# Performance work log

Hardware: AMD Instinct MI355X
Metric: run time of the kernel (lower is better)

## Reference

```python
import jax, jax.numpy as jnp
import numpy as np
import math

D_MODEL = 512
EXPAND = 1
D_INNER = EXPAND * D_MODEL          # 512
HALF = D_INNER // 2                 # 256 per-branch channels
D_STATE = D_MODEL // 4 * EXPAND     # 128 (overrides d_state arg in __init__)
DT_RANK = math.ceil(D_MODEL / 16)   # 32
D_CONV = 4


def _dwconv_same(x, w):
    # x: (B, C, L), w: (C, 1, k); torch padding='same' for k=4 -> pad (left=1, right=2)
    k = w.shape[-1]
    total = k - 1
    left = total // 2
    return jax.lax.conv_general_dilated(
        x, w, window_strides=(1,), padding=[(left, total - left)],
        feature_group_count=w.shape[0], dimension_numbers=("NCH", "OIH", "NCH"))


def _sparse_approx(m):
    thr = jnp.max(m) * 0.1
    return jnp.sign(m) * jax.nn.relu(jnp.abs(m) - thr)


def _selective_scan(u, delta, A, Bc, Cc, D):
    # u, delta: (B, d, L); A: (d, n); Bc, Cc: (B, n, L); D: (d,)
    dT = jnp.moveaxis(delta, 2, 0)   # (L, B, d)
    uT = jnp.moveaxis(u, 2, 0)       # (L, B, d)
    BT = jnp.moveaxis(Bc, 2, 0)      # (L, B, n)
    CT = jnp.moveaxis(Cc, 2, 0)      # (L, B, n)

    def step(h, inputs):
        d_t, u_t, b_t, c_t = inputs                      # (B,d),(B,d),(B,n),(B,n)
        dA = jnp.exp(d_t[..., None] * A)                 # (B, d, n)
        dBu = d_t[..., None] * b_t[:, None, :] * u_t[..., None]
        h = dA * h + dBu                                 # (B, d, n)
        y = jnp.einsum("bdn,bn->bd", h, c_t)
        return h, y

    h0 = jnp.zeros((u.shape[0], u.shape[1], A.shape[1]), dtype=u.dtype)
    _, ys = jax.lax.scan(step, h0, (dT, uT, BT, CT))     # ys: (L, B, d)
    y = jnp.moveaxis(ys, 0, 2)                           # (B, d, L)
    return y + u * D[:, None]


def _branch(inph, in_w, cx_w, cz_w, xproj_w, dt_w, dt_b, out_w, A, D):
    # inph: (B, L, d_model)
    xz = jnp.swapaxes(inph @ in_w.T, 1, 2)   # (B, d_inner, L)
    x, z = xz[:, :HALF], xz[:, HALF:]
    x = jax.nn.silu(_dwconv_same(x, cx_w))   # (B, half, L); conv bias is False (True//2==0)
    z = jax.nn.silu(_dwconv_same(z, cz_w))
    x_dbl = jnp.swapaxes(x, 1, 2) @ xproj_w.T        # (B, L, dt_rank + 2n)
    dt = x_dbl[..., :DT_RANK] @ dt_w.T               # (B, L, half)
    dt = jnp.swapaxes(dt, 1, 2)                      # (B, half, L)
    Bc = jnp.swapaxes(x_dbl[..., DT_RANK:DT_RANK + D_STATE], 1, 2)   # (B, n, L)
    Cc = jnp.swapaxes(x_dbl[..., DT_RANK + D_STATE:], 1, 2)          # (B, n, L)
    Bc = _sparse_approx(Bc)
    Cc = _sparse_approx(Cc)
    delta = jax.nn.softplus(dt + dt_b[None, :, None])
    y = _selective_scan(x, delta, A, Bc, Cc, D)
    out = jnp.concatenate([y, z], axis=1)            # (B, d_inner, L)
    return jnp.swapaxes(out, 1, 2) @ out_w.T         # (B, L, d_model)


def setup_inputs() -> dict:
    key = jax.random.key(0)
    ks = jax.random.split(key, 16)
    B, L = 2, 2048
    s = lambda fan: 1.0 / np.sqrt(fan)

    inp = jax.random.normal(ks[0], (B, 2 * D_MODEL, L), jnp.float32)

    in_proj_w = jax.random.uniform(ks[1], (D_INNER, D_MODEL), jnp.float32, -s(D_MODEL), s(D_MODEL))
    x_proj_w = jax.random.uniform(ks[2], (DT_RANK + 2 * D_STATE, HALF), jnp.float32, -s(HALF), s(HALF))
    dt_init_std = DT_RANK ** (-0.5)
    dt_proj_w = jax.random.uniform(ks[3], (HALF, DT_RANK), jnp.float32, -dt_init_std, dt_init_std)
    out_proj_w = jax.random.uniform(ks[4], (D_MODEL, D_INNER), jnp.float32, -s(D_INNER), s(D_INNER))

    in_proj_2_w = jax.random.uniform(ks[5], (D_INNER, D_MODEL), jnp.float32, -s(D_MODEL), s(D_MODEL))
    x_proj_2_w = jax.random.uniform(ks[6], (DT_RANK + 2 * D_STATE, HALF), jnp.float32, -s(HALF), s(HALF))
    dt_proj_2_w = jax.random.uniform(ks[7], (HALF, DT_RANK), jnp.float32, -dt_init_std, dt_init_std)
    out_proj_2_w = jax.random.uniform(ks[8], (D_MODEL, D_INNER), jnp.float32, -s(D_INNER), s(D_INNER))

    # dt bias init: inverse-softplus of dt ~ LogUniform(1e-3, 1e-1), floor 1e-4
    def inv_softplus_dt(k):
        u = jax.random.uniform(k, (HALF,), jnp.float32)
        dt = jnp.exp(u * (np.log(0.1) - np.log(0.001)) + np.log(0.001))
        dt = jnp.clip(dt, 1e-4, None)
        return dt + jnp.log(-jnp.expm1(-dt))
    dt_proj_b = inv_softplus_dt(ks[9])
    dt_proj_2_b = inv_softplus_dt(ks[10])

    cs = 1.0 / np.sqrt(D_CONV)  # depthwise conv fan_in = 1*k
    conv_x_w = jax.random.uniform(ks[11], (HALF, 1, D_CONV), jnp.float32, -cs, cs)
    conv_z_w = jax.random.uniform(ks[12], (HALF, 1, D_CONV), jnp.float32, -cs, cs)
    conv_x_2_w = jax.random.uniform(ks[13], (HALF, 1, D_CONV), jnp.float32, -cs, cs)
    conv_z_2_w = jax.random.uniform(ks[14], (HALF, 1, D_CONV), jnp.float32, -cs, cs)

    A_log = jnp.log(jnp.broadcast_to(jnp.arange(1, D_STATE + 1, dtype=jnp.float32), (HALF, D_STATE)))
    D = jnp.ones((HALF,), jnp.float32)
    epsilon = jnp.array([0.01], jnp.float32)

    return dict(inp=inp, in_proj_w=in_proj_w, conv_x_w=conv_x_w, conv_z_w=conv_z_w,
                x_proj_w=x_proj_w, dt_proj_w=dt_proj_w, dt_proj_b=dt_proj_b, out_proj_w=out_proj_w,
                in_proj_2_w=in_proj_2_w, conv_x_2_w=conv_x_2_w, conv_z_2_w=conv_z_2_w,
                x_proj_2_w=x_proj_2_w, dt_proj_2_w=dt_proj_2_w, dt_proj_2_b=dt_proj_2_b,
                out_proj_2_w=out_proj_2_w, A_log=A_log, D=D, epsilon=epsilon)


def reference(inp, in_proj_w, conv_x_w, conv_z_w, x_proj_w, dt_proj_w, dt_proj_b, out_proj_w,
              in_proj_2_w, conv_x_2_w, conv_z_2_w, x_proj_2_w, dt_proj_2_w, dt_proj_2_b,
              out_proj_2_w, A_log, D, epsilon):
    # inp: (B, 2*d_model, L) -> split along dim 1, permute to (B, L, d_model)
    inpx = jnp.swapaxes(inp[:, :D_MODEL, :], 1, 2)
    inpy = jnp.swapaxes(inp[:, D_MODEL:, :], 1, 2)

    A_base = (1.0 + epsilon[0]) * (-jnp.exp(A_log))
    A1 = _sparse_approx(A_base)        # branch 1
    A2 = _sparse_approx(A1)            # branch 2 sparsifies the already-sparsified A

    out1 = _branch(inpx, in_proj_w, conv_x_w, conv_z_w, x_proj_w, dt_proj_w, dt_proj_b, out_proj_w, A1, D)
    out2 = _branch(inpy, in_proj_2_w, conv_x_2_w, conv_z_2_w, x_proj_2_w, dt_proj_2_w, dt_proj_2_b, out_proj_2_w, A2, D)
    return out1, out2
```

## Files before the change

### kernel.cpp

```cpp
#include <hip/hip_runtime.h>
#include <math.h>

constexpr int B_    = 2;
constexpr int L_    = 2048;
constexpr int NROW  = B_ * L_;
constexpr int MROW  = 2 * NROW;
constexpr int HALF_ = 256;
constexpr int DS_   = 128;

constexpr float LOG2E = 1.4426950408889634f;

constexpr size_t OFF_MINP = 0;
constexpr size_t OFF_BCMX = 32;
constexpr size_t OFF_XZ   = 64;
constexpr size_t OFF_YT   = OFF_XZ + (size_t)MROW * 256;
constexpr size_t OFF_XDBL = OFF_XZ + (size_t)MROW * 512;
constexpr size_t OFF_XS   = OFF_XDBL + (size_t)MROW * 288;
constexpr size_t OFF_BS   = OFF_XS  + (size_t)MROW * 256;
constexpr size_t OFF_CS   = OFF_BS  + (size_t)2 * NROW * 128;
constexpr size_t OFF_DTT  = OFF_CS  + (size_t)2 * NROW * 128;
constexpr size_t OFF_DUT  = OFF_DTT + (size_t)2 * 256 * 4096;
constexpr size_t OFF_UDT  = OFF_DUT + (size_t)2 * 256 * 4096;
constexpr size_t FLOAT_END = OFF_UDT + (size_t)2 * 256 * 4096;

constexpr size_t HOFF_XINH = 0;
constexpr size_t HOFF_XINL = HOFF_XINH + (size_t)MROW * 512;
constexpr size_t HOFF_YZH  = HOFF_XINH;
constexpr size_t HOFF_YZL  = HOFF_XINL;
constexpr size_t HOFF_XSH  = HOFF_XINL + (size_t)MROW * 512;
constexpr size_t HOFF_XSL  = HOFF_XSH  + (size_t)MROW * 256;
constexpr size_t HOFF_INWH = HOFF_XSL  + (size_t)MROW * 256;
constexpr size_t HOFF_INWL = HOFF_INWH + 524288;
constexpr size_t HOFF_XWH  = HOFF_INWL + 524288;
constexpr size_t HOFF_XWL  = HOFF_XWH  + 147456;
constexpr size_t HOFF_OUTWH= HOFF_XWL  + 147456;
constexpr size_t HOFF_OUTWL= HOFF_OUTWH+ 524288;

constexpr size_t WST_IN = 262144;
constexpr size_t WST_X  = 73728;

constexpr int PRE_MINA = 32;
constexpr int PRE_WSPL = (1196032 + 255) / 256;
constexpr int PRE_TIN  = 64 * 16 * 4;
constexpr int PRE_BLOCKS = PRE_MINA + PRE_WSPL + PRE_TIN;

typedef __bf16 bf16x8 __attribute__((ext_vector_type(8)));
typedef float  f32x4  __attribute__((ext_vector_type(4)));

__device__ __forceinline__ unsigned short bf16rn(float x) {
    unsigned u = __float_as_uint(x);
    unsigned r = (u + 0x7FFFu + ((u >> 16) & 1u)) >> 16;
    return (unsigned short)r;
}
__device__ __forceinline__ void split2(float x, unsigned short& h, unsigned short& l) {
    h = bf16rn(x);
    float hf = __uint_as_float(((unsigned)h) << 16);
    l = bf16rn(x - hf);
}

__device__ __forceinline__ float shrinkf(float v, float thr) {
    float a = fabsf(v) - thr;
    a = fmaxf(a, 0.0f);
    float r = copysignf(a, v);
    return (v == 0.0f) ? 0.0f : r;
}
__device__ __forceinline__ float siluf(float v) { return v / (1.0f + __expf(-v)); }
__device__ __forceinline__ float softplusf(float v) {
    return fmaxf(v, 0.0f) + log1pf(__expf(-fabsf(v)));
}
__device__ __forceinline__ float rlanef(float v, int l) {
    return __int_as_float(__builtin_amdgcn_readlane(__float_as_int(v), l));
}
__device__ __forceinline__ unsigned fkey(float f) {
    unsigned u = __float_as_uint(f);
    return (u >> 31) ? ~u : (u | 0x80000000u);
}
__device__ __forceinline__ float funkey(unsigned k) {
    unsigned u = (k >> 31) ? (k & 0x7FFFFFFFu) : ~k;
    return __uint_as_float(u);
}

__global__ __launch_bounds__(256) void pre_all(const float* __restrict__ A_log,
                                               const float* __restrict__ inp,
                                               const float* __restrict__ in_w0,
                                               const float* __restrict__ in_w1,
                                               const float* __restrict__ outw0,
                                               const float* __restrict__ outw1,
                                               const float* __restrict__ xw0,
                                               const float* __restrict__ xw1,
                                               float* __restrict__ ws,
                                               unsigned* __restrict__ bcmax,
                                               unsigned short* __restrict__ hb) {
    int bid = blockIdx.x;
    int tid = threadIdx.x;
    if (bid < PRE_MINA) {
        __shared__ float sbuf[8];
        int i = bid * 1024 + tid * 4;
        float4 v = *(const float4*)(A_log + i);
        float mv = fminf(fminf(v.x, v.y), fminf(v.z, v.w));
        #pragma unroll
        for (int off = 32; off > 0; off >>= 1) mv = fminf(mv, __shfl_xor(mv, off));
        if ((tid & 63) == 0) sbuf[tid >> 6] = mv;
        __syncthreads();
        if (tid == 0) {
            float r = fminf(fminf(sbuf[0], sbuf[1]), fminf(sbuf[2], sbuf[3]));
            ws[OFF_MINP + bid] = r;
        }
        if (bid == 0 && tid < 4) bcmax[tid] = 0u;
    } else if (bid < PRE_MINA + PRE_WSPL) {
        int i = (bid - PRE_MINA) * 256 + tid;
        if (i >= 1196032) return;
        const float* src;
        size_t hbase, lbase;
        int off;
        if (i < 1048576) {
            int t = i >> 18;
            off = i & 262143;
            src = (t == 0) ? in_w0 : (t == 1) ? in_w1 : (t == 2) ? outw0 : outw1;
            if (t < 2) { hbase = HOFF_INWH + (size_t)t * WST_IN;  lbase = HOFF_INWL + (size_t)t * WST_IN; }
            else       { hbase = HOFF_OUTWH + (size_t)(t - 2) * WST_IN; lbase = HOFF_OUTWL + (size_t)(t - 2) * WST_IN; }
        } else {
            int j = i - 1048576;
            int t = (j < (int)WST_X) ? 0 : 1;
            off = j - t * (int)WST_X;
            src = t ? xw1 : xw0;
            hbase = HOFF_XWH + (size_t)t * WST_X;
            lbase = HOFF_XWL + (size_t)t * WST_X;
        }
        unsigned short h, l;
        split2(src[off], h, l);
        hb[hbase + off] = h;
        hb[lbase + off] = l;
    } else {
        __shared__ float tile[32][33];
        int idx = bid - PRE_MINA - PRE_WSPL;
        int bx = idx & 63;
        int by = (idx >> 6) & 15;
        int z  = idx >> 10;
        int br = z >> 1;
        int b  = z & 1;
        int t0 = bx * 32;
        int m0 = by * 32;
        int tx = tid & 31;
        int ty = tid >> 5;
        #pragma unroll
        for (int k = 0; k < 4; k++) {
            tile[ty + 8 * k][tx] =
                inp[((size_t)b * 1024 + br * 512 + m0 + ty + 8 * k) * L_ + t0 + tx];
        }
        __syncthreads();
        #pragma unroll
        for (int k = 0; k < 4; k++) {
            size_t dst = ((size_t)br * NROW + (size_t)b * L_ + t0 + ty + 8 * k) * 512 + m0 + tx;
            unsigned short h, l;
            split2(tile[tx][ty + 8 * k], h, l);
            hb[HOFF_XINH + dst] = h;
            hb[HOFF_XINL + dst] = l;
        }
    }
}

template <int NGUARD, int DOMAX>
__global__ __launch_bounds__(256) void gemm_mfma(const unsigned short* __restrict__ Ah,
                                                 const unsigned short* __restrict__ Al, int lda,
                                                 const unsigned short* __restrict__ WhB,
                                                 const unsigned short* __restrict__ WlB,
                                                 size_t wstride,
                                                 float* __restrict__ C, int ldc,
                                                 int N, int K,
                                                 unsigned* __restrict__ bcmax) {
    __shared__ __align__(16) unsigned short sAh[128 * 40];
    __shared__ __align__(16) unsigned short sAl[128 * 40];
    __shared__ __align__(16) unsigned short sBh[64 * 40];
    __shared__ __align__(16) unsigned short sBl[64 * 40];
    int tid  = threadIdx.x;
    int wid  = tid >> 6;
    int lane = tid & 63;
    int fr   = lane & 15;
    int kg   = lane >> 4;
    int mblk = blockIdx.y * 128;
    int nblk = blockIdx.x * 64;
    int br   = (mblk >= NROW) ? 1 : 0;
    const unsigned short* Wh = WhB + (size_t)br * wstride;
    const unsigned short* Wl = WlB + (size_t)br * wstride;
    int srow = tid >> 2;
    int skp  = (tid & 3) * 8;
    bool brow_ok = (!NGUARD) || ((nblk + srow) < N);

    const unsigned short* pA0 = Ah + (size_t)(mblk + srow) * lda + skp;
    const unsigned short* pA1 = Ah + (size_t)(mblk + 64 + srow) * lda + skp;
    const unsigned short* pL0 = Al + (size_t)(mblk + srow) * lda + skp;
    const unsigned short* pL1 = Al + (size_t)(mblk + 64 + srow) * lda + skp;
    const unsigned short* pBh = Wh + (size_t)(nblk + srow) * K + skp;
    const unsigned short* pBl = Wl + (size_t)(nblk + srow) * K + skp;

    f32x4 acc[2][4] = {};

    uint4 rah0 = *(const uint4*)(pA0);
    uint4 rah1 = *(const uint4*)(pA1);
    uint4 ral0 = *(const uint4*)(pL0);
    uint4 ral1 = *(const uint4*)(pL1);
    uint4 rbh = {0, 0, 0, 0}, rbl = {0, 0, 0, 0};
    if (brow_ok) {
        rbh = *(const uint4*)(pBh);
        rbl = *(const uint4*)(pBl);
    }

    for (int k0 = 0; k0 < K; k0 += 32) {
        __syncthreads();
        *(uint4*)(sAh + srow * 40 + skp) = rah0;
        *(uint4*)(sAh + (64 + srow) * 40 + skp) = rah1;
        *(uint4*)(sAl + srow * 40 + skp) = ral0;
        *(uint4*)(sAl + (64 + srow) * 40 + skp) = ral1;
        *(uint4*)(sBh + srow * 40 + skp) = rbh;
        *(uint4*)(sBl + srow * 40 + skp) = rbl;
        __syncthreads();

        int kn = k0 + 32;
        if (kn < K) {
            rah0 = *(const uint4*)(pA0 + kn);
            rah1 = *(const uint4*)(pA1 + kn);
            ral0 = *(const uint4*)(pL0 + kn);
            ral1 = *(const uint4*)(pL1 + kn);
            if (brow_ok) {
                rbh = *(const uint4*)(pBh + kn);
                rbl = *(const uint4*)(pBl + kn);
            }
        }

        bf16x8 ah0 = *(const bf16x8*)(sAh + (wid * 32 + fr) * 40 + kg * 8);
        bf16x8 ah1 = *(const bf16x8*)(sAh + (wid * 32 + 16 + fr) * 40 + kg * 8);
        bf16x8 al0 = *(const bf16x8*)(sAl + (wid * 32 + fr) * 40 + kg * 8);
        bf16x8 al1 = *(const bf16x8*)(sAl + (wid * 32 + 16 + fr) * 40 + kg * 8);
        #pragma unroll
        for (int nt = 0; nt < 4; nt++) {
            bf16x8 bh = *(const bf16x8*)(sBh + (nt * 16 + fr) * 40 + kg * 8);
            bf16x8 bl = *(const bf16x8*)(sBl + (nt * 16 + fr) * 40 + kg * 8);
            acc[0][nt] = __builtin_amdgcn_mfma_f32_16x16x32_bf16(ah0, bh, acc[0][nt], 0, 0, 0);
            acc[0][nt] = __builtin_amdgcn_mfma_f32_16x16x32_bf16(ah0, bl, acc[0][nt], 0, 0, 0);
            acc[0][nt] = __builtin_amdgcn_mfma_f32_16x16x32_bf16(al0, bh, acc[0][nt], 0, 0, 0);
            acc[1][nt] = __builtin_amdgcn_mfma_f32_16x16x32_bf16(ah1, bh, acc[1][nt], 0, 0, 0);
            acc[1][nt] = __builtin_amdgcn_mfma_f32_16x16x32_bf16(ah1, bl, acc[1][nt], 0, 0, 0);
            acc[1][nt] = __builtin_amdgcn_mfma_f32_16x16x32_bf16(al1, bh, acc[1][nt], 0, 0, 0);
        }
    }
    #pragma unroll
    for (int mt = 0; mt < 2; mt++) {
        #pragma unroll
        for (int nt = 0; nt < 4; nt++) {
            int col = nblk + nt * 16 + fr;
            if (NGUARD && col >= N) continue;
            #pragma unroll
            for (int r = 0; r < 4; r++) {
                int row = mblk + wid * 32 + mt * 16 + kg * 4 + r;
                C[(size_t)row * ldc + col] = acc[mt][nt][r];
            }
        }
    }
    if (DOMAX) {
        float mb = -INFINITY, mc = -INFINITY;
        #pragma unroll
        for (int nt = 0; nt < 4; nt++) {
            int c16 = nblk + nt * 16;
            if (c16 >= 32 && c16 < 160) {
                #pragma unroll
                for (int mt = 0; mt < 2; mt++)
                    #pragma unroll
                    for (int r = 0; r < 4; r++) mb = fmaxf(mb, acc[mt][nt][r]);
            } else if (c16 >= 160 && c16 < 288) {
                #pragma unroll
                for (int mt = 0; mt < 2; mt++)
                    #pragma unroll
                    for (int r = 0; r < 4; r++) mc = fmaxf(mc, acc[mt][nt][r]);
            }
        }
        #pragma unroll
        for (int off = 32; off > 0; off >>= 1) {
            mb = fmaxf(mb, __shfl_xor(mb, off));
            mc = fmaxf(mc, __shfl_xor(mc, off));
        }
        if (lane == 0) {
            if (mb > -INFINITY) atomicMax(bcmax + 2 * br,     fkey(mb));
            if (mc > -INFINITY) atomicMax(bcmax + 2 * br + 1, fkey(mc));
        }
    }
}

__global__ __launch_bounds__(256) void conv_silu_kernel(const float* __restrict__ xz,
                                                        float* __restrict__ xs,
                                                        unsigned short* __restrict__ xsh,
                                                        unsigned short* __restrict__ xsl,
                                                        unsigned short* __restrict__ yzh,
                                                        unsigned short* __restrict__ yzl,
                                                        const float* __restrict__ wx0,
                                                        const float* __restrict__ wx1,
                                                        const float* __restrict__ wz0,
                                                        const float* __restrict__ wz1) {
    int gid = blockIdx.x * 256 + threadIdx.x;
    int c4  = (gid & 63) << 2;
    int row = gid >> 6;
    int br  = row >> 12;
    int t   = row & (L_ - 1);
    const float* wx = br ? wx1 : wx0;
    const float* wz = br ? wz1 : wz0;
    float4 wxv[4], wzv[4];
    #pragma unroll
    for (int k = 0; k < 4; k++) {
        wxv[k] = *(const float4*)(wx + (c4 + k) * 4);
        wzv[k] = *(const float4*)(wz + (c4 + k) * 4);
    }
    float4 ax = {0, 0, 0, 0}, az = {0, 0, 0, 0};
    #pragma unroll
    for (int j = 0; j < 4; j++) {
        int tt = t + j - 1;
        if (tt >= 0 && tt < L_) {
            const float* p = xz + (size_t)(row + j - 1) * 512;
            float4 vx = *(const float4*)(p + c4);
            float4 vz = *(const float4*)(p + 256 + c4);
            ax.x = fmaf(vx.x, ((const float*)&wxv[0])[j], ax.x);
            ax.y = fmaf(vx.y, ((const float*)&wxv[1])[j], ax.y);
            ax.z = fmaf(vx.z, ((const float*)&wxv[2])[j], ax.z);
            ax.w = fmaf(vx.w, ((const float*)&wxv[3])[j], ax.w);
            az.x = fmaf(vz.x, ((const float*)&wzv[0])[j], az.x);
            az.y = fmaf(vz.y, ((const float*)&wzv[1])[j], az.y);
            az.z = fmaf(vz.z, ((const float*)&wzv[2])[j], az.z);
            az.w = fmaf(vz.w, ((const float*)&wzv[3])[j], az.w);
        }
    }
    float4 sx, sz;
    sx.x = siluf(ax.x); sx.y = siluf(ax.y); sx.z = siluf(ax.z); sx.w = siluf(ax.w);
    sz.x = siluf(az.x); sz.y = siluf(az.y); sz.z = siluf(az.z); sz.w = siluf(az.w);
    *(float4*)(xs + (size_t)row * 256 + c4) = sx;
    ushort4 hx, lx, hz, lz;
    split2(sx.x, hx.x, lx.x); split2(sx.y, hx.y, lx.y);
    split2(sx.z, hx.z, lx.z); split2(sx.w, hx.w, lx.w);
    split2(sz.x, hz.x, lz.x); split2(sz.y, hz.y, lz.y);
    split2(sz.z, hz.z, lz.z); split2(sz.w, hz.w, lz.w);
    *(ushort4*)(xsh + (size_t)row * 256 + c4) = hx;
    *(ushort4*)(xsl + (size_t)row * 256 + c4) = lx;
    *(ushort4*)(yzh + (size_t)row * 512 + 256 + c4) = hz;
    *(ushort4*)(yzl + (size_t)row * 512 + 256 + c4) = lz;
}

__global__ __launch_bounds__(256) void dtprep_shrink(const float* __restrict__ A, int lda,
                                                     const float* __restrict__ W0,
                                                     const float* __restrict__ W1,
                                                     const float* __restrict__ b0,
                                                     const float* __restrict__ b1,
                                                     const float* __restrict__ xs,
                                                     const float* __restrict__ Dvec,
                                                     float* __restrict__ dtT,
                                                     float* __restrict__ duT,
                                                     float* __restrict__ udT,
                                                     const unsigned* __restrict__ bcmax,
                                                     float* __restrict__ Bs,
                                                     float* __restrict__ Cs) {
    __shared__ float As[16][68];
    __shared__ float Ws[16][68];
    __shared__ float tb[64 * 68];
    int tid = threadIdx.x;
    int kk = tid & 15;
    int rr = tid >> 4;
    int mblk = blockIdx.y * 64;
    int nblk = blockIdx.x * 64;
    int br = (mblk >= NROW) ? 1 : 0;
    const float* W    = br ? W1 : W0;
    const float* bias = br ? b1 : b0;
    float acc[4][4] = {};
    for (int k0 = 0; k0 < 32; k0 += 16) {
        #pragma unroll
        for (int j = 0; j < 4; j++) {
            As[kk][rr + 16 * j] = A[(size_t)(mblk + rr + 16 * j) * lda + k0 + kk];
        }
        #pragma unroll
        for (int j = 0; j < 4; j++) {
            Ws[kk][rr + 16 * j] = W[(size_t)(nblk + rr + 16 * j) * 32 + k0 + kk];
        }
        __syncthreads();
        int ty = tid >> 4;
        int tx = tid & 15;
        #pragma unroll
        for (int kq = 0; kq < 16; kq++) {
            float a0 = As[kq][ty * 4 + 0];
            float a1 = As[kq][ty * 4 + 1];
            float a2 = As[kq][ty * 4 + 2];
            float a3 = As[kq][ty * 4 + 3];
            float v0 = Ws[kq][tx * 4 + 0];
            float v1 = Ws[kq][tx * 4 + 1];
            float v2 = Ws[kq][tx * 4 + 2];
            float v3 = Ws[kq][tx * 4 + 3];
            acc[0][0] = fmaf(a0, v0, acc[0][0]); acc[0][1] = fmaf(a0, v1, acc[0][1]);
            acc[0][2] = fmaf(a0, v2, acc[0][2]); acc[0][3] = fmaf(a0, v3, acc[0][3]);
            acc[1][0] = fmaf(a1, v0, acc[1][0]); acc[1][1] = fmaf(a1, v1, acc[1][1]);
            acc[1][2] = fmaf(a1, v2, acc[1][2]); acc[1][3] = fmaf(a1, v3, acc[1][3]);
            acc[2][0] = fmaf(a2, v0, acc[2][0]); acc[2][1] = fmaf(a2, v1, acc[2][1]);
            acc[2][2] = fmaf(a2, v2, acc[2][2]); acc[2][3] = fmaf(a2, v3, acc[2][3]);
            acc[3][0] = fmaf(a3, v0, acc[3][0]); acc[3][1] = fmaf(a3, v1, acc[3][1]);
            acc[3][2] = fmaf(a3, v2, acc[3][2]); acc[3][3] = fmaf(a3, v3, acc[3][3]);
        }
        __syncthreads();
    }
    int ty = tid >> 4;
    int tx = tid & 15;
    float dlt[4][4], uu[4][4];
    #pragma unroll
    for (int i = 0; i < 4; i++) {
        int m = mblk + ty * 4 + i;
        #pragma unroll
        for (int j = 0; j < 4; j++) {
            int n = nblk + tx * 4 + j;
            dlt[i][j] = softplusf(acc[i][j] + bias[n]);
            uu[i][j]  = xs[(size_t)m * 256 + n];
        }
    }
    float Dv[4];
    #pragma unroll
    for (int j = 0; j < 4; j++) Dv[j] = Dvec[nblk + tx * 4 + j];

    int mlocbase = mblk & (NROW - 1);
    int nrd  = tid >> 2;
    int mc   = (tid & 3) * 4;
    size_t obase = ((size_t)br * 256 + nblk + nrd) * 4096 + mlocbase;
    #pragma unroll
    for (int pass = 0; pass < 3; pass++) {
        __syncthreads();
        #pragma unroll
        for (int i = 0; i < 4; i++) {
            #pragma unroll
            for (int j = 0; j < 4; j++) {
                float v = (pass == 0) ? dlt[i][j] * LOG2E
                        : (pass == 1) ? dlt[i][j] * uu[i][j]
                                      : uu[i][j] * Dv[j];
                tb[(tx * 4 + j) * 68 + ty * 4 + i] = v;
            }
        }
        __syncthreads();
        float* dst = (pass == 0) ? dtT : (pass == 1) ? duT : udT;
        #pragma unroll
        for (int it = 0; it < 4; it++) {
            int cc = mc + it * 16;
            float4 v = *(const float4*)(tb + nrd * 68 + cc);
            *(float4*)(dst + obase + cc) = v;
        }
    }
    {
        int q = blockIdx.x;
        int isC = q >> 1;
        int cbase = (q & 1) * 64;
        int xoff = isC ? (160 + cbase) : (32 + cbase);
        float thr = 0.1f * funkey(bcmax[2 * br + isC]);
        float* dstArr = isC ? Cs : Bs;
        int r = tid >> 2;
        int c0 = (tid & 3) * 16;
        const float* src = A + (size_t)(mblk + r) * lda + xoff + c0;
        float* dp = dstArr + (size_t)(mblk + r) * 128 + cbase + c0;
        #pragma unroll
        for (int i = 0; i < 16; i += 4) {
            float4 v = *(const float4*)(src + i);
            float4 o;
            o.x = shrinkf(v.x, thr);
            o.y = shrinkf(v.y, thr);
            o.z = shrinkf(v.z, thr);
            o.w = shrinkf(v.w, thr);
            *(float4*)(dp + i) = o;
        }
    }
}

__global__ __launch_bounds__(128) void scan3_kernel(float* __restrict__ ws,
                                                    const float* __restrict__ A_log,
                                                    const float* __restrict__ eps) {
    int blk  = blockIdx.x;
    int xcd  = blk & 7;
    int slot = blk >> 3;
    int combo = xcd >> 1;
    int d  = (xcd & 1) * 128 + slot;
    int br = combo >> 1;
    int b  = combo & 1;
    int tid = threadIdx.x;
    int lt  = tid & 63;

    float pv = ws[OFF_MINP + (tid & 31)];
    #pragma unroll
    for (int off = 16; off > 0; off >>= 1) pv = fminf(pv, __shfl_xor(pv, off));
    float e  = 1.0f + eps[0];
    float m1 = -e * __expf(pv);
    float t1 = 0.1f * m1;
    float t2 = 0.1f * shrinkf(m1, t1);
    float base = -e * __expf(A_log[d * 128 + tid]);
    float a = shrinkf(base, t1);
    if (br) a = shrinkf(a, t2);

    size_t dchain = ((size_t)br * 256 + d) * 4096 + (size_t)b * L_;
    const float* dtT = ws + OFF_DTT + dchain;
    const float* duT = ws + OFF_DUT + dchain;
    const float* udT = ws + OFF_UDT + dchain;
    const float* Bp  = ws + OFF_BS + ((size_t)br * NROW + (size_t)b * L_) * 128 + tid;
    const float* Cp  = ws + OFF_CS + ((size_t)br * NROW + (size_t)b * L_) * 128 + tid;
    float*       yTp = ws + OFF_YT + dchain;

    __shared__ float red[64 * 132];
    __shared__ float comb[64];

    float h = 0.0f;

    float Bb[2][8], Cb[2][8];
    float dt_c = dtT[lt];
    float du_c = duT[lt];
    float ud_c = udT[lt];
    float dt_n = 0.f, du_n = 0.f, ud_n = 0.f;
    #pragma unroll
    for (int j = 0; j < 8; j++) { Bb[0][j] = Bp[(size_t)j * 128];       Cb[0][j] = Cp[(size_t)j * 128]; }
    #pragma unroll
    for (int j = 0; j < 8; j++) { Bb[1][j] = Bp[(size_t)(8 + j) * 128]; Cb[1][j] = Cp[(size_t)(8 + j) * 128]; }

    for (int c = 0; c < 32; c++) {
        if (c < 31) {
            dt_n = dtT[(c + 1) * 64 + lt];
            du_n = duT[(c + 1) * 64 + lt];
            ud_n = udT[(c + 1) * 64 + lt];
        }
        #pragma unroll
        for (int m = 0; m < 8; m++) {
            const int cur = m & 1;
            #pragma unroll
            for (int j = 0; j < 8; j++) {
                const int tl = m * 8 + j;
                float dt2 = rlanef(dt_c, tl);
                float du  = rlanef(du_c, tl);
                float ev = __builtin_amdgcn_exp2f(dt2 * a);
                h = fmaf(ev, h, du * Bb[cur][j]);
                red[tl * 132 + tid] = h * Cb[cur][j];
            }
            int nb = c * 8 + m + 2;
            if (nb < 256) {
                #pragma unroll
                for (int j = 0; j < 8; j++) {
                    Bb[cur][j] = Bp[((size_t)nb * 8 + j) * 128];
                    Cb[cur][j] = Cp[((size_t)nb * 8 + j) * 128];
                }
            }
        }
        __syncthreads();
        {
            const float* rp = &red[(tid & 63) * 132 + (tid >> 6) * 64];
            float s0 = 0.f, s1 = 0.f, s2 = 0.f, s3 = 0.f;
            #pragma unroll
            for (int i = 0; i < 64; i += 4) {
                float4 v = *(const float4*)(rp + i);
                s0 += v.x; s1 += v.y; s2 += v.z; s3 += v.w;
            }
            float part = (s0 + s1) + (s2 + s3);
            if (tid >= 64) comb[tid - 64] = part;
            __syncthreads();
            if (tid < 64) yTp[c * 64 + tid] = part + comb[tid] + ud_c;
        }
        __syncthreads();
        dt_c = dt_n;
        du_c = du_n;
        ud_c = ud_n;
    }
}

__global__ __launch_bounds__(256) void transpose_yz_kernel(const float* __restrict__ yT,
                                                           unsigned short* __restrict__ yzh,
                                                           unsigned short* __restrict__ yzl) {
    __shared__ float tile[32][33];
    int br = blockIdx.z;
    int m0 = blockIdx.x * 32;
    int n0 = blockIdx.y * 32;
    int tx = threadIdx.x;
    int ty = threadIdx.y;
    #pragma unroll
    for (int k = 0; k < 4; k++) {
        tile[ty + 8 * k][tx] = yT[((size_t)br * 256 + m0 + ty + 8 * k) * 4096 + n0 + tx];
    }
    __syncthreads();
    #pragma unroll
    for (int k = 0; k < 4; k++) {
        size_t dst = ((size_t)br * NROW + n0 + ty + 8 * k) * 512 + m0 + tx;
        unsigned short h, l;
        split2(tile[tx][ty + 8 * k], h, l);
        yzh[dst] = h; yzl[dst] = l;
    }
}

extern "C" void kernel_launch(void* const* d_in, const int* in_sizes, int n_in,
                              void* d_out, int out_size, void* d_ws, size_t ws_size,
                              hipStream_t stream) {
    const float* inp   = (const float*)d_in[0];
    const float* in_w[2]  = {(const float*)d_in[1],  (const float*)d_in[8]};
    const float* cxw[2]   = {(const float*)d_in[2],  (const float*)d_in[9]};
    const float* czw[2]   = {(const float*)d_in[3],  (const float*)d_in[10]};
    const float* xw[2]    = {(const float*)d_in[4],  (const float*)d_in[11]};
    const float* dtw[2]   = {(const float*)d_in[5],  (const float*)d_in[12]};
    const float* dtb[2]   = {(const float*)d_in[6],  (const float*)d_in[13]};
    const float* outw[2]  = {(const float*)d_in[7],  (const float*)d_in[14]};
    const float* A_log = (const float*)d_in[15];
    const float* Dvec  = (const float*)d_in[16];
    const float* eps   = (const float*)d_in[17];
    float* out = (float*)d_out;
    float* ws  = (float*)d_ws;
    unsigned short* hb = (unsigned short*)(ws + FLOAT_END);
    unsigned* bcmax = (unsigned*)(ws + OFF_BCMX);

    pre_all<<<PRE_BLOCKS, 256, 0, stream>>>(
        A_log, inp, in_w[0], in_w[1], outw[0], outw[1], xw[0], xw[1],
        ws, bcmax, hb);

    gemm_mfma<0, 0><<<dim3(512 / 64, MROW / 128), 256, 0, stream>>>(
        hb + HOFF_XINH, hb + HOFF_XINL, 512,
        hb + HOFF_INWH, hb + HOFF_INWL, WST_IN,
        ws + OFF_XZ, 512, 512, 512, nullptr);

    conv_silu_kernel<<<(MROW * 64) / 256, 256, 0, stream>>>(
        ws + OFF_XZ, ws + OFF_XS, hb + HOFF_XSH, hb + HOFF_XSL,
        hb + HOFF_YZH, hb + HOFF_YZL, cxw[0], cxw[1], czw[0], czw[1]);

    gemm_mfma<1, 1><<<dim3((288 + 63) / 64, MROW / 128), 256, 0, stream>>>(
        hb + HOFF_XSH, hb + HOFF_XSL, 256,
        hb + HOFF_XWH, hb + HOFF_XWL, WST_X,
        ws + OFF_XDBL, 288, 288, 256, bcmax);

    dtprep_shrink<<<dim3(4, MROW / 64), 256, 0, stream>>>(
        ws + OFF_XDBL, 288, dtw[0], dtw[1], dtb[0], dtb[1],
        ws + OFF_XS, Dvec,
        ws + OFF_DTT, ws + OFF_DUT, ws + OFF_UDT,
        bcmax, ws + OFF_BS, ws + OFF_CS);

    scan3_kernel<<<dim3(1024), 128, 0, stream>>>(ws, A_log, eps);

    transpose_yz_kernel<<<dim3(256 / 32, NROW / 32, 2), dim3(32, 8), 0, stream>>>(
        ws + OFF_YT, hb + HOFF_YZH, hb + HOFF_YZL);

    gemm_mfma<0, 0><<<dim3(512 / 64, MROW / 128), 256, 0, stream>>>(
        hb + HOFF_YZH, hb + HOFF_YZL, 512,
        hb + HOFF_OUTWH, hb + HOFF_OUTWL, WST_IN,
        out, 512, 512, 512, nullptr);
}
```

Baseline: 326.6 us.

## Run selective scan with one wave per chain, two states per lane

```diff
diff --git a/kernel.cpp b/kernel.cpp
--- a/kernel.cpp
+++ b/kernel.cpp
@@ -467,98 +467,108 @@
     }
 }
 
-__global__ __launch_bounds__(128) void scan3_kernel(float* __restrict__ ws,
-                                                    const float* __restrict__ A_log,
-                                                    const float* __restrict__ eps) {
-    int blk  = blockIdx.x;
-    int xcd  = blk & 7;
-    int slot = blk >> 3;
-    int combo = xcd >> 1;
-    int d  = (xcd & 1) * 128 + slot;
-    int br = combo >> 1;
-    int b  = combo & 1;
-    int tid = threadIdx.x;
-    int lt  = tid & 63;
-
-    float pv = ws[OFF_MINP + (tid & 31)];
+__global__ __launch_bounds__(64, 1) void scan4_kernel(float* __restrict__ ws,
+                                                      const float* __restrict__ A_log,
+                                                      const float* __restrict__ eps) {
+    int g  = blockIdx.x;
+    int d  = g >> 2;
+    int br = (g >> 1) & 1;
+    int b  = g & 1;
+    int lane = threadIdx.x;
+
+    float pv = ws[OFF_MINP + (lane & 31)];
     #pragma unroll
     for (int off = 16; off > 0; off >>= 1) pv = fminf(pv, __shfl_xor(pv, off));
     float e  = 1.0f + eps[0];
     float m1 = -e * __expf(pv);
     float t1 = 0.1f * m1;
     float t2 = 0.1f * shrinkf(m1, t1);
-    float base = -e * __expf(A_log[d * 128 + tid]);
-    float a = shrinkf(base, t1);
-    if (br) a = shrinkf(a, t2);
+    float base0 = -e * __expf(A_log[d * 128 + lane]);
+    float base1 = -e * __expf(A_log[d * 128 + 64 + lane]);
+    float a0 = shrinkf(base0, t1);
+    float a1 = shrinkf(base1, t1);
+    if (br) { a0 = shrinkf(a0, t2); a1 = shrinkf(a1, t2); }
 
     size_t dchain = ((size_t)br * 256 + d) * 4096 + (size_t)b * L_;
-    const float* dtT = ws + OFF_DTT + dchain;
-    const float* duT = ws + OFF_DUT + dchain;
-    const float* udT = ws + OFF_UDT + dchain;
-    const float* Bp  = ws + OFF_BS + ((size_t)br * NROW + (size_t)b * L_) * 128 + tid;
-    const float* Cp  = ws + OFF_CS + ((size_t)br * NROW + (size_t)b * L_) * 128 + tid;
-    float*       yTp = ws + OFF_YT + dchain;
-
-    __shared__ float red[64 * 132];
-    __shared__ float comb[64];
-
-    float h = 0.0f;
-
-    float Bb[2][8], Cb[2][8];
-    float dt_c = dtT[lt];
-    float du_c = duT[lt];
-    float ud_c = udT[lt];
-    float dt_n = 0.f, du_n = 0.f, ud_n = 0.f;
-    #pragma unroll
-    for (int j = 0; j < 8; j++) { Bb[0][j] = Bp[(size_t)j * 128];       Cb[0][j] = Cp[(size_t)j * 128]; }
-    #pragma unroll
-    for (int j = 0; j < 8; j++) { Bb[1][j] = Bp[(size_t)(8 + j) * 128]; Cb[1][j] = Cp[(size_t)(8 + j) * 128]; }
-
+    const float* dtp = ws + OFF_DTT + dchain;
+    const float* dup = ws + OFF_DUT + dchain;
+    const float* udp = ws + OFF_UDT + dchain;
+    size_t bcrow = ((size_t)br * NROW + (size_t)b * L_) * 128;
+    const float* Bq0 = ws + OFF_BS + bcrow + lane;
+    const float* Bq1 = ws + OFF_BS + bcrow + 64 + lane;
+    const float* Cq0 = ws + OFF_CS + bcrow + lane;
+    const float* Cq1 = ws + OFF_CS + bcrow + 64 + lane;
+    float* yTp = ws + OFF_YT + dchain;
+
+    __shared__ float red[32 * 66];
+
+    float h0 = 0.0f, h1 = 0.0f;
+    float Bb0[4][8], Bb1[4][8], Cb0[4][8], Cb1[4][8];
+
+    #pragma unroll
+    for (int q = 0; q < 4; q++) {
+        #pragma unroll
+        for (int j = 0; j < 8; j++) {
+            Bb0[q][j] = Bq0[(size_t)j * 128];
+            Bb1[q][j] = Bq1[(size_t)j * 128];
+            Cb0[q][j] = Cq0[(size_t)j * 128];
+            Cb1[q][j] = Cq1[(size_t)j * 128];
+        }
+        Bq0 += 1024; Bq1 += 1024; Cq0 += 1024; Cq1 += 1024;
+    }
+
+    float dt_c = dtp[lane];
+    float du_c = dup[lane];
+    float dt_n = 0.0f, du_n = 0.0f;
+
+    #pragma unroll 1
     for (int c = 0; c < 32; c++) {
-        if (c < 31) {
-            dt_n = dtT[(c + 1) * 64 + lt];
-            du_n = duT[(c + 1) * 64 + lt];
-            ud_n = udT[(c + 1) * 64 + lt];
-        }
+        if (c < 31) { dt_n = dtp[64 + lane]; du_n = dup[64 + lane]; }
+        dtp += 64; dup += 64;
         #pragma unroll
         for (int m = 0; m < 8; m++) {
-            const int cur = m & 1;
+            const int cur = m & 3;
             #pragma unroll
             for (int j = 0; j < 8; j++) {
                 const int tl = m * 8 + j;
+                const int tloc = (m & 3) * 8 + j;
                 float dt2 = rlanef(dt_c, tl);
                 float du  = rlanef(du_c, tl);
-                float ev = __builtin_amdgcn_exp2f(dt2 * a);
-                h = fmaf(ev, h, du * Bb[cur][j]);
-                red[tl * 132 + tid] = h * Cb[cur][j];
+                float ev0 = __builtin_amdgcn_exp2f(dt2 * a0);
+                float ev1 = __builtin_amdgcn_exp2f(dt2 * a1);
+                h0 = fmaf(ev0, h0, du * Bb0[cur][j]);
+                h1 = fmaf(ev1, h1, du * Bb1[cur][j]);
+                red[tloc * 66 + lane] = fmaf(h1, Cb1[cur][j], h0 * Cb0[cur][j]);
             }
-            int nb = c * 8 + m + 2;
-            if (nb < 256) {
+            #pragma unroll
+            for (int j = 0; j < 8; j++) {
+                Bb0[cur][j] = Bq0[(size_t)j * 128];
+                Bb1[cur][j] = Bq1[(size_t)j * 128];
+                Cb0[cur][j] = Cq0[(size_t)j * 128];
+                Cb1[cur][j] = Cq1[(size_t)j * 128];
+            }
+            Bq0 += 1024; Bq1 += 1024; Cq0 += 1024; Cq1 += 1024;
+            if ((m & 3) == 3) {
+                __builtin_amdgcn_wave_barrier();
+                int t    = lane & 31;
+                int half = lane >> 5;
+                const float* rp = red + t * 66 + half * 32;
+                float s0 = 0.0f, s1 = 0.0f;
                 #pragma unroll
-                for (int j = 0; j < 8; j++) {
-                    Bb[cur][j] = Bp[((size_t)nb * 8 + j) * 128];
-                    Cb[cur][j] = Cp[((size_t)nb * 8 + j) * 128];
+                for (int i = 0; i < 32; i += 2) {
+                    float2 v = *(const float2*)(rp + i);
+                    s0 += v.x; s1 += v.y;
                 }
+                float tot = s0 + s1;
+                tot += __shfl_xor(tot, 32);
+                int c32 = c * 2 + (m >> 2);
+                float ud = udp[(size_t)c32 * 32 + t];
+                if (lane < 32) yTp[(size_t)c32 * 32 + t] = tot + ud;
+                __builtin_amdgcn_wave_barrier();
             }
         }
-        __syncthreads();
-        {
-            const float* rp = &red[(tid & 63) * 132 + (tid >> 6) * 64];
-            float s0 = 0.f, s1 = 0.f, s2 = 0.f, s3 = 0.f;
-            #pragma unroll
-            for (int i = 0; i < 64; i += 4) {
-                float4 v = *(const float4*)(rp + i);
-                s0 += v.x; s1 += v.y; s2 += v.z; s3 += v.w;
-            }
-            float part = (s0 + s1) + (s2 + s3);
-            if (tid >= 64) comb[tid - 64] = part;
-            __syncthreads();
-            if (tid < 64) yTp[c * 64 + tid] = part + comb[tid] + ud_c;
-        }
-        __syncthreads();
         dt_c = dt_n;
         du_c = du_n;
-        ud_c = ud_n;
     }
 }
 
@@ -628,7 +638,7 @@
         ws + OFF_DTT, ws + OFF_DUT, ws + OFF_UDT,
         bcmax, ws + OFF_BS, ws + OFF_CS);
 
-    scan3_kernel<<<dim3(1024), 128, 0, stream>>>(ws, A_log, eps);
+    scan4_kernel<<<dim3(1024), 64, 0, stream>>>(ws, A_log, eps);
 
     transpose_yz_kernel<<<dim3(256 / 32, NROW / 32, 2), dim3(32, 8), 0, stream>>>(
         ws + OFF_YT, hb + HOFF_YZH, hb + HOFF_YZL);
```

After: 393.4 us. 20.5% more time.

## Make scan reduction wave-local and load dt/du as uniform scalars per step

Applied to the files above, without the earlier changes.

```diff
diff --git a/kernel.cpp b/kernel.cpp
--- a/kernel.cpp
+++ b/kernel.cpp
@@ -467,7 +467,7 @@
     }
 }
 
-__global__ __launch_bounds__(128) void scan3_kernel(float* __restrict__ ws,
+__global__ __launch_bounds__(128) void scan7_kernel(float* __restrict__ ws,
                                                     const float* __restrict__ A_log,
                                                     const float* __restrict__ eps) {
     int blk  = blockIdx.x;
@@ -479,6 +479,7 @@
     int b  = combo & 1;
     int tid = threadIdx.x;
     int lt  = tid & 63;
+    int half = tid >> 6;
 
     float pv = ws[OFF_MINP + (tid & 31)];
     #pragma unroll
@@ -500,37 +501,34 @@
     float*       yTp = ws + OFF_YT + dchain;
 
     __shared__ float red[64 * 132];
-    __shared__ float comb[64];
+    __shared__ float comb[2][64];
 
     float h = 0.0f;
 
     float Bb[2][8], Cb[2][8];
-    float dt_c = dtT[lt];
-    float du_c = duT[lt];
-    float ud_c = udT[lt];
-    float dt_n = 0.f, du_n = 0.f, ud_n = 0.f;
     #pragma unroll
     for (int j = 0; j < 8; j++) { Bb[0][j] = Bp[(size_t)j * 128];       Cb[0][j] = Cp[(size_t)j * 128]; }
     #pragma unroll
     for (int j = 0; j < 8; j++) { Bb[1][j] = Bp[(size_t)(8 + j) * 128]; Cb[1][j] = Cp[(size_t)(8 + j) * 128]; }
 
     for (int c = 0; c < 32; c++) {
-        if (c < 31) {
-            dt_n = dtT[(c + 1) * 64 + lt];
-            du_n = duT[(c + 1) * 64 + lt];
-            ud_n = udT[(c + 1) * 64 + lt];
-        }
+        float ud_c = 0.0f;
+        if (tid < 64) ud_c = udT[c * 64 + tid];
         #pragma unroll
         for (int m = 0; m < 8; m++) {
             const int cur = m & 1;
+            float dts[8], dus[8];
+            #pragma unroll
+            for (int j = 0; j < 8; j++) {
+                dts[j] = dtT[c * 64 + m * 8 + j];
+                dus[j] = duT[c * 64 + m * 8 + j];
+            }
             #pragma unroll
             for (int j = 0; j < 8; j++) {
                 const int tl = m * 8 + j;
-                float dt2 = rlanef(dt_c, tl);
-                float du  = rlanef(du_c, tl);
-                float ev = __builtin_amdgcn_exp2f(dt2 * a);
-                h = fmaf(ev, h, du * Bb[cur][j]);
-                red[tl * 132 + tid] = h * Cb[cur][j];
+                float ev = __builtin_amdgcn_exp2f(dts[j] * a);
+                h = fmaf(ev, h, dus[j] * Bb[cur][j]);
+                red[tl * 132 + half * 66 + lt] = h * Cb[cur][j];
             }
             int nb = c * 8 + m + 2;
             if (nb < 256) {
@@ -541,24 +539,21 @@
                 }
             }
         }
-        __syncthreads();
+        __builtin_amdgcn_wave_barrier();
         {
-            const float* rp = &red[(tid & 63) * 132 + (tid >> 6) * 64];
-            float s0 = 0.f, s1 = 0.f, s2 = 0.f, s3 = 0.f;
+            const float* rp = &red[lt * 132 + half * 66];
+            float s0 = 0.0f, s1 = 0.0f;
             #pragma unroll
-            for (int i = 0; i < 64; i += 4) {
-                float4 v = *(const float4*)(rp + i);
-                s0 += v.x; s1 += v.y; s2 += v.z; s3 += v.w;
-            }
-            float part = (s0 + s1) + (s2 + s3);
-            if (tid >= 64) comb[tid - 64] = part;
+            for (int i = 0; i < 64; i += 2) {
+                float2 v = *(const float2*)(rp + i);
+                s0 += v.x; s1 += v.y;
+            }
+            float part = s0 + s1;
+            if (half) comb[c & 1][lt] = part;
             __syncthreads();
-            if (tid < 64) yTp[c * 64 + tid] = part + comb[tid] + ud_c;
-        }
-        __syncthreads();
-        dt_c = dt_n;
-        du_c = du_n;
-        ud_c = ud_n;
+            if (!half) yTp[c * 64 + lt] = part + comb[c & 1][lt] + ud_c;
+        }
+        __builtin_amdgcn_wave_barrier();
     }
 }
 
@@ -628,7 +623,7 @@
         ws + OFF_DTT, ws + OFF_DUT, ws + OFF_UDT,
         bcmax, ws + OFF_BS, ws + OFF_CS);
 
-    scan3_kernel<<<dim3(1024), 128, 0, stream>>>(ws, A_log, eps);
+    scan7_kernel<<<dim3(1024), 128, 0, stream>>>(ws, A_log, eps);
 
     transpose_yz_kernel<<<dim3(256 / 32, NROW / 32, 2), dim3(32, 8), 0, stream>>>(
         ws + OFF_YT, hb + HOFF_YZH, hb + HOFF_YZL);
```

Measured after the change: 351.7 us. +7.7%, slower.
